# Optimization experiments

Measured on AMD Instinct MI355X. Metric: run time of the kernel, lower is better.

The kernel has to match this reference:

```python
import jax, jax.numpy as jnp
import numpy as np

B, T, V, E, DC, H = 128, 25, 10000, 512, 512, 512
N0 = H + E + DC  # layer-0 concat width
N1 = 2 * H       # layer-1 concat width


def setup_inputs() -> dict:
    key = jax.random.key(0)
    ks = jax.random.split(key, 12)
    def w(k, n):
        return jax.random.normal(k, (n, H), dtype=jnp.float32) / np.float32(np.sqrt(n))
    return {
        "tokens": jax.random.randint(ks[0], (B, T), 0, V),
        "processed_cnn_features": jax.random.normal(ks[1], (B, DC), dtype=jnp.float32),
        "initial_hidden_state": jnp.zeros((2, B, H), dtype=jnp.float32),
        "embedding": jax.random.normal(ks[2], (V, E), dtype=jnp.float32) * 0.1,
        "Wu0": w(ks[3], N0), "Wr0": w(ks[4], N0), "Wc0": w(ks[5], N0),
        "bu0": jnp.zeros((H,), jnp.float32), "br0": jnp.zeros((H,), jnp.float32), "bc0": jnp.zeros((H,), jnp.float32),
        "Wu1": w(ks[6], N1), "Wr1": w(ks[7], N1), "Wc1": w(ks[8], N1),
        "bu1": jnp.zeros((H,), jnp.float32), "br1": jnp.zeros((H,), jnp.float32), "bc1": jnp.zeros((H,), jnp.float32),
        "Wout": jax.random.normal(ks[9], (H, V), dtype=jnp.float32) / np.float32(np.sqrt(H)),
        "bout": jnp.zeros((V,), jnp.float32),
    }


def gru_step(x, h, Wu, bu, Wr, br, Wc, bc):
    xh = jnp.concatenate([x, h], axis=1)
    u = jax.nn.sigmoid(xh @ Wu + bu)
    r = jax.nn.sigmoid(xh @ Wr + br)
    cand = jnp.tanh(jnp.concatenate([x, r * h], axis=1) @ Wc + bc)
    return u * h + (1.0 - u) * cand


def reference(tokens, processed_cnn_features, initial_hidden_state, embedding,
              Wu0, Wr0, Wc0, bu0, br0, bc0,
              Wu1, Wr1, Wc1, bu1, br1, bc1,
              Wout, bout):
    emb = embedding[tokens]              # [B, T, E]
    emb_t = jnp.transpose(emb, (1, 0, 2))  # [T, B, E]

    def step(carry, e_t):
        h0, h1 = carry
        x0 = jnp.concatenate([e_t, processed_cnn_features], axis=1)  # [B, E+DC]
        h0 = gru_step(x0, h0, Wu0, bu0, Wr0, br0, Wc0, bc0)
        h1 = gru_step(h0, h1, Wu1, bu1, Wr1, br1, Wc1, bc1)
        logits = h1 @ Wout + bout  # [B, V]
        return (h0, h1), logits

    (h0, h1), logits_seq = jax.lax.scan(step, (initial_hidden_state[0], initial_hidden_state[1]), emb_t)
    logits = jnp.transpose(logits_seq, (1, 0, 2))  # [B, T, V]
    final_hidden = jnp.stack([h0, h1])             # [2, B, H]
    return logits, final_hidden
```

## Files before the change

### kernel.cpp

```cpp
#include <hip/hip_runtime.h>

#define T_ 25
#define V_ 10000
#define NWG_ 192

#define R_P3 0
#define R_P1 1
#define R_P4 2
#define R_P2 3

typedef short bf16x8 __attribute__((ext_vector_type(8)));
typedef float f32x4 __attribute__((ext_vector_type(4)));

__device__ __forceinline__ short f2bf(float x) {
  union { float f; unsigned u; } v; v.f = x;
  unsigned r = (v.u + 0x7fffu + ((v.u >> 16) & 1u)) >> 16;
  return (short)r;
}
__device__ __forceinline__ float sigm(float z) { return 1.f / (1.f + __expf(-z)); }
__device__ __forceinline__ float tanhfast(float z) {
  float e = __expf(2.f * z);
  return 1.f - 2.f / (e + 1.f);
}

__device__ __forceinline__ void gload_lds16(const void* g, void* l) {
  __builtin_amdgcn_global_load_lds((const __attribute__((address_space(1))) void*)g,
                                   (__attribute__((address_space(3))) void*)l, 16, 0, 0);
}

__device__ __forceinline__ void vwait0() { asm volatile("s_waitcnt vmcnt(0)" ::: "memory"); }
__device__ __forceinline__ void vwait_n(int n) {
  switch (n) {
    case 0:  asm volatile("s_waitcnt vmcnt(0)"  ::: "memory"); break;
    case 8:  asm volatile("s_waitcnt vmcnt(8)"  ::: "memory"); break;
    case 16: asm volatile("s_waitcnt vmcnt(16)" ::: "memory"); break;
    default: asm volatile("s_waitcnt vmcnt(0)"  ::: "memory"); break;
  }
}
__device__ __forceinline__ void ncload16(bf16x8* d, const short* p) {
  asm volatile("global_load_dwordx4 %0, %1, off" : "=v"(*d) : "v"(p) : "memory");
}
__device__ __forceinline__ void cstoref(float* p, float v) {
  asm volatile("global_store_dword %0, %1, off sc0 sc1" :: "v"(p), "v"(v) : "memory");
}
__device__ __forceinline__ void cstores(short* p, int v) {
  asm volatile("global_store_short %0, %1, off sc0 sc1" :: "v"(p), "v"(v) : "memory");
}

__device__ __forceinline__ int FL(int row, int col) {
  return (((col >> 5) * 8 + (row >> 4)) << 9) | (((row & 15) | (((col >> 3) & 3) << 4)) << 3) | (col & 7);
}

__device__ __forceinline__ void setflag(int* bar, int role, int wg, int val) {
  vwait0();
  __syncthreads();
  if (threadIdx.x == 0) {
    int* wp = bar + role * 256 + wg;
    asm volatile("global_store_dword %0, %1, off sc0 sc1" :: "v"(wp), "v"(val) : "memory");
  }
}
__device__ __forceinline__ void waitflag(int* bar, int role, int cnt, int need) {
  if (threadIdx.x < 64) {
    int idx = (int)threadIdx.x < cnt ? (int)threadIdx.x : cnt - 1;
    const int* wp = bar + role * 256 + idx;
    for (;;) {
      int v;
      asm volatile("global_load_dword %0, %1, off sc0 sc1" : "=v"(v) : "v"(wp) : "memory");
      asm volatile("s_waitcnt vmcnt(0)" ::: "memory");
      if (__all(v >= need)) break;
      __builtin_amdgcn_s_sleep(1);
    }
  }
  __syncthreads();
}

struct TJob { const float* src; short* dst; int R, C, t0; };
struct TJobs { TJob j[10]; };

__global__ void tcast_all(TJobs J) {
  __shared__ float t[32][33];
  int bid = blockIdx.x;
  int ji = 0;
  while (ji < 9 && bid >= J.j[ji + 1].t0) ji++;
  const float* src = J.j[ji].src;
  short* dst = J.j[ji].dst;
  int R = J.j[ji].R, C = J.j[ji].C;
  int rel = bid - J.j[ji].t0;
  int ctiles = (C + 31) >> 5;
  int rt0 = (rel / ctiles) * 32, ct0 = (rel % ctiles) * 32;
  int tx = threadIdx.x, ty = threadIdx.y;
#pragma unroll
  for (int i = 0; i < 4; i++) {
    int r = rt0 + ty + i * 8, c = ct0 + tx;
    if (r < R && c < C) t[ty + i * 8][tx] = src[(size_t)r * C + c];
  }
  __syncthreads();
#pragma unroll
  for (int i = 0; i < 4; i++) {
    int c = ct0 + ty + i * 8, r = rt0 + tx;
    if (r < R && c < C) dst[(size_t)c * R + r] = f2bf(t[tx][ty + i * 8]);
  }
}

__global__ void build_x0(const int* __restrict__ tok, const float* __restrict__ emb,
                         const float* __restrict__ cnn, short* __restrict__ X0) {
  int row = blockIdx.x;
  int t = row >> 7, b = row & 127;
  int tk = tok[b * T_ + t];
  const float* er = emb + (size_t)tk * 512;
  short* dst = X0 + (size_t)row * 1024;
  for (int i = threadIdx.x; i < 1024; i += 256)
    dst[i] = f2bf(i < 512 ? er[i] : cnn[b * 512 + (i - 512)]);
}

__global__ void init_h(const float* __restrict__ ihs, float* h0f0, float* h1f0, short* H0) {
  int i = blockIdx.x * 256 + threadIdx.x;
  if (i < 65536) {
    int b = i >> 9, h = i & 511;
    float v0 = ihs[i], v1 = ihs[65536 + i];
    h0f0[i] = v0; h1f0[i] = v1;
    H0[FL(b, h)] = f2bf(v0);
    H0[FL(b, 512 + h)] = f2bf(v1);
  }
}

struct RP {
  short *Hb, *XCb, *RHb, *H1all;
  float *u0b, *u1b, *h0b, *h1b;
  const float *A0;
  const short *Whur0T, *Whc0T, *W1urT, *Wc1T;
  const float *bu1, *br1, *bc1;
  float *outp;
  int *bar;
};

template<int NKS>
__device__ __forceinline__ void wload(const short* __restrict__ Wt, int n0, int lane, bf16x8* wfr) {
  const short* p = Wt + (size_t)(n0 + (lane & 15)) * (NKS * 32) + ((lane >> 4) * 8);
#pragma unroll
  for (int ks = 0; ks < NKS; ks++) wfr[ks] = *(const bf16x8*)(p + (size_t)ks * 32);
}

template<int NKS, bool SPLIT>
__device__ __forceinline__ void kcompute(const short* __restrict__ Alo, const short* __restrict__ Ahi,
                                         int rb0, int lane, const bf16x8* __restrict__ wfr, f32x4* acc) {
  const short* aplo = Alo + rb0 * 512 + lane * 8;
  const short* aphi = Ahi + rb0 * 512 + lane * 8;
  constexpr int NCH = NKS / 4;
  constexpr int DEPTH = NCH < 3 ? NCH : 3;
  bf16x8 s0[4][4], s1[4][4];
#pragma unroll
  for (int c = 0; c < DEPTH; c++)
#pragma unroll
    for (int j = 0; j < 4; j++) {
      int ks = c * 4 + j;
      const short* ap = (SPLIT && ks >= NKS / 2) ? aphi : aplo;
      ncload16(&s0[c & 3][j], ap + ks * 4096);
      ncload16(&s1[c & 3][j], ap + ks * 4096 + 512);
    }
#pragma unroll
  for (int c = 0; c < NCH; c++) {
    const int issued = (DEPTH + c < NCH) ? DEPTH + c : NCH;
    vwait_n((issued - c - 1) * 8);
    __builtin_amdgcn_sched_barrier(0);
#pragma unroll
    for (int j = 0; j < 4; j++) {
      int ks = c * 4 + j;
      acc[ks & 1]       = __builtin_amdgcn_mfma_f32_16x16x32_bf16(s0[c & 3][j], wfr[ks], acc[ks & 1], 0, 0, 0);
      acc[2 + (ks & 1)] = __builtin_amdgcn_mfma_f32_16x16x32_bf16(s1[c & 3][j], wfr[ks], acc[2 + (ks & 1)], 0, 0, 0);
    }
    if (DEPTH + c < NCH) {
      const int nc = DEPTH + c;
#pragma unroll
      for (int j = 0; j < 4; j++) {
        int ks = nc * 4 + j;
        const short* ap = (SPLIT && ks >= NKS / 2) ? aphi : aplo;
        ncload16(&s0[nc & 3][j], ap + ks * 4096);
        ncload16(&s1[nc & 3][j], ap + ks * 4096 + 512);
      }
    }
  }
}

__global__ __launch_bounds__(256, 1) void recurrence(RP p) {
  const int bid = blockIdx.x;
  const int m8 = bid & 7;
  const int k = ((bid & 127) >> 3) * 4 + (m8 & 3);
  const int role = (bid < 128) ? ((m8 < 4) ? R_P3 : R_P1) : ((m8 < 4) ? R_P4 : R_P2);
  const int tid = threadIdx.x, wv = tid >> 6, lane = tid & 63;
  const int lr = lane & 15, lg = lane >> 4;
  int* bar = p.bar;
  const int nt = k >> 1, mh = k & 1;
  const int colb = nt * 32 + (wv & 1) * 16;
  const int rb0 = mh * 4 + (wv >> 1) * 2;
  const int col = colb + lr;

  if (role == R_P3) {
    bf16x8 wfr[32]; wload<32>(p.W1urT, colb, lane, wfr);
    for (int s = 0; s < T_; s++) {
      waitflag(bar, R_P2, 32, s + 1);
      if (s >= 1) waitflag(bar, R_P4, 32, s);
      const short* Hs1 = p.Hb + (size_t)(s + 1) * 131072;
      const short* Hs  = p.Hb + (size_t)s * 131072;
      f32x4 acc[4] = {};
      kcompute<32, true>(Hs1, Hs, rb0, lane, wfr, acc);
      f32x4 am[2] = { acc[0] + acc[1], acc[2] + acc[3] };
      short* xc = p.XCb + (size_t)s * 131072;
      const float* h1s = p.h1b + (size_t)s * 65536;
      float* u1s = p.u1b + (size_t)s * 65536;
#pragma unroll
      for (int m = 0; m < 2; m++)
#pragma unroll
        for (int i = 0; i < 4; i++) {
          int row = (rb0 + m) * 16 + lg * 4 + i;
          if (colb < 512) {
            cstoref(&u1s[row * 512 + col], sigm(am[m][i] + p.bu1[col]));
          } else {
            float sg = sigm(am[m][i] + p.br1[col - 512]);
            cstores(&xc[FL(row, col)], f2bf(sg * h1s[row * 512 + (col - 512)]));
          }
        }
      setflag(bar, R_P3, k, s + 1);
    }
  } else if (role == R_P1) {
    bf16x8 wfr[16]; wload<16>(p.Whur0T, colb, lane, wfr);
    for (int s = 0; s < T_; s++) {
      if (s >= 1) waitflag(bar, R_P2, 32, s);
      const short* Hs = p.Hb + (size_t)s * 131072;
      f32x4 acc[4] = {};
      kcompute<16, false>(Hs, Hs, rb0, lane, wfr, acc);
      f32x4 am[2] = { acc[0] + acc[1], acc[2] + acc[3] };
      const float* a0s = p.A0 + (size_t)s * 196608;
      const float* h0s = p.h0b + (size_t)s * 65536;
      float* u0s = p.u0b + (size_t)s * 65536;
      short* rh = p.RHb + (size_t)s * 65536;
#pragma unroll
      for (int m = 0; m < 2; m++)
#pragma unroll
        for (int i = 0; i < 4; i++) {
          int row = (rb0 + m) * 16 + lg * 4 + i;
          if (colb < 512) {
            cstoref(&u0s[row * 512 + col], sigm(am[m][i] + a0s[row * 1536 + col]));
          } else {
            float sg = sigm(am[m][i] + a0s[row * 1536 + col]);
            cstores(&rh[FL(row, col - 512)], f2bf(sg * h0s[row * 512 + (col - 512)]));
          }
        }
      setflag(bar, R_P1, k, s + 1);
    }
  } else if (role == R_P4) {
    bf16x8 wfr[32]; wload<32>(p.Wc1T, colb, lane, wfr);
    for (int s = 0; s < T_; s++) {
      waitflag(bar, R_P3, 64, s + 1);
      waitflag(bar, R_P2, 32, s + 1);
      const short* xc = p.XCb + (size_t)s * 131072;
      f32x4 acc[4] = {};
      kcompute<32, false>(xc, xc, rb0, lane, wfr, acc);
      f32x4 am[2] = { acc[0] + acc[1], acc[2] + acc[3] };
      const float* u1s = p.u1b + (size_t)s * 65536;
      const float* h1s = p.h1b + (size_t)s * 65536;
      float* h1d = p.h1b + (size_t)(s + 1) * 65536;
      short* xh = p.Hb + (size_t)(s + 1) * 131072;
#pragma unroll
      for (int m = 0; m < 2; m++)
#pragma unroll
        for (int i = 0; i < 4; i++) {
          int row = (rb0 + m) * 16 + lg * 4 + i;
          float cc = tanhfast(am[m][i] + p.bc1[col]);
          float u = u1s[row * 512 + col], h = h1s[row * 512 + col];
          float hn = u * h + (1.f - u) * cc;
          cstoref(&h1d[row * 512 + col], hn);
          short hb = f2bf(hn);
          cstores(&xh[FL(row, 512 + col)], hb);
          p.H1all[(size_t)s * 65536 + row * 512 + col] = hb;
          if (s == T_ - 1) p.outp[32000000 + 65536 + row * 512 + col] = hn;
        }
      setflag(bar, R_P4, k, s + 1);
    }
  } else {
    bf16x8 wfr[16]; wload<16>(p.Whc0T, colb, lane, wfr);
    for (int s = 0; s < T_; s++) {
      waitflag(bar, R_P1, 64, s + 1);
      const short* rh = p.RHb + (size_t)s * 65536;
      f32x4 acc[4] = {};
      kcompute<16, false>(rh, rh, rb0, lane, wfr, acc);
      f32x4 am[2] = { acc[0] + acc[1], acc[2] + acc[3] };
      const float* a0s = p.A0 + (size_t)s * 196608;
      const float* u0s = p.u0b + (size_t)s * 65536;
      const float* h0s = p.h0b + (size_t)s * 65536;
      float* h0d = p.h0b + (size_t)(s + 1) * 65536;
      short* xh  = p.Hb + (size_t)(s + 1) * 131072;
      short* xcw = p.XCb + (size_t)s * 131072;
#pragma unroll
      for (int m = 0; m < 2; m++)
#pragma unroll
        for (int i = 0; i < 4; i++) {
          int row = (rb0 + m) * 16 + lg * 4 + i;
          float c = tanhfast(am[m][i] + a0s[row * 1536 + 1024 + col]);
          float u = u0s[row * 512 + col], h = h0s[row * 512 + col];
          float hn = u * h + (1.f - u) * c;
          cstoref(&h0d[row * 512 + col], hn);
          short hb = f2bf(hn);
          cstores(&xh[FL(row, col)], hb);
          cstores(&xcw[FL(row, col)], hb);
          if (s == T_ - 1) p.outp[32000000 + row * 512 + col] = hn;
        }
      setflag(bar, R_P2, k, s + 1);
    }
  }
}

struct GP {
  const short* A; const short* Bt;
  int lda, ldb, N, K;
  const float* bias0; const float* bias1; const float* bias2;
  float* fdst;
  float* outp; const float* bout;
};

template<int BM, int BN, int VAR>
__device__ __forceinline__ void gemm_core(const GP& p, short* la, short* lb, int bm, int bn, short* smem) {
  const int tid = threadIdx.x;
  const int wave = tid >> 6, lane = tid & 63;
  const int wm = wave >> 1, wn = wave & 1;
  constexpr int WM = BM / 2, WN = BN / 2;
  constexpr int MF = WM / 16, NF = WN / 16;
  const int lr = lane & 15, lg = lane >> 4;
  const short* Abase = p.A + (size_t)bm * BM * p.lda;
  const short* Bbase = p.Bt + (size_t)bn * BN * p.ldb;
  const int bnmax = p.N - bn * BN;
  f32x4 acc[MF][NF] = {};
  const int nkb = p.K >> 6;

  auto stA = [&](int buf, int k0) {
    constexpr int NI = BM / 32;
#pragma unroll
    for (int j = 0; j < NI; j++) {
      int glin = j * 256 + tid;
      int row = glin >> 3, gc = glin & 7;
      int gcs = gc ^ (row & 7);
      gload_lds16(Abase + (size_t)row * p.lda + k0 + gcs * 8,
                  &la[buf * BM * 64 + j * 2048 + wave * 512]);
    }
  };
  auto stB = [&](int buf, int k0) {
    constexpr int NI = BN / 32;
#pragma unroll
    for (int j = 0; j < NI; j++) {
      int glin = j * 256 + tid;
      int row = glin >> 3, gc = glin & 7;
      int gcs = gc ^ (row & 7);
      int rc = row < bnmax ? row : bnmax - 1;
      gload_lds16(Bbase + (size_t)rc * p.ldb + k0 + gcs * 8,
                  &lb[buf * BN * 64 + j * 2048 + wave * 512]);
    }
  };

  stA(0, 0); stB(0, 0);
  __syncthreads();
  int buf = 0;
  for (int kb = 0; kb < nkb; kb++) {
    if (kb + 1 < nkb) { stA(buf ^ 1, (kb + 1) * 64); stB(buf ^ 1, (kb + 1) * 64); }
    bf16x8 af[2][MF], bfr[2][NF];
#pragma unroll
    for (int ks = 0; ks < 2; ks++) {
#pragma unroll
      for (int m = 0; m < MF; m++) {
        int ar = wm * WM + m * 16 + lr;
        af[ks][m] = *(const bf16x8*)&la[buf * BM * 64 + (ar * 8 + ((ks * 4 + lg) ^ (ar & 7))) * 8];
      }
#pragma unroll
      for (int n = 0; n < NF; n++) {
        int br = wn * WN + n * 16 + lr;
        bfr[ks][n] = *(const bf16x8*)&lb[buf * BN * 64 + (br * 8 + ((ks * 4 + lg) ^ (br & 7))) * 8];
      }
    }
#pragma unroll
    for (int ks = 0; ks < 2; ks++)
#pragma unroll
      for (int m = 0; m < MF; m++)
#pragma unroll
        for (int n = 0; n < NF; n++)
          acc[m][n] = __builtin_amdgcn_mfma_f32_16x16x32_bf16(af[ks][m], bfr[ks][n], acc[m][n], 0, 0, 0);
    __syncthreads();
    buf ^= 1;
  }

  if constexpr (VAR == 0) {
#pragma unroll
    for (int m = 0; m < MF; m++)
#pragma unroll
      for (int n = 0; n < NF; n++)
#pragma unroll
        for (int i = 0; i < 4; i++) {
          int row = bm * BM + wm * WM + m * 16 + lg * 4 + i;
          int col = bn * BN + wn * WN + n * 16 + lr;
          if (col >= p.N) continue;
          float bias = col < 512 ? p.bias0[col] : (col < 1024 ? p.bias1[col - 512] : p.bias2[col - 1024]);
          p.fdst[(size_t)row * 1536 + col] = acc[m][n][i] + bias;
        }
  } else {
    float* fs = (float*)smem;
#pragma unroll
    for (int m = 0; m < MF; m++)
#pragma unroll
      for (int n = 0; n < NF; n++)
#pragma unroll
        for (int i = 0; i < 4; i++) {
          int lrow = wm * WM + m * 16 + lg * 4 + i;
          int lcol = wn * WN + n * 16 + lr;
          int col = bn * BN + lcol;
          fs[lrow * 128 + lcol] = acc[m][n][i] + (col < p.N ? p.bout[col] : 0.f);
        }
    __syncthreads();
#pragma unroll
    for (int j = 0; j < 16; j++) {
      int idx = j * 256 + tid;
      int r = idx >> 5, c4 = (idx & 31) << 2;
      int gr = bm * BM + r;
      int tt = gr >> 7, b = gr & 127;
      int col = bn * BN + c4;
      if (col < p.N) {
        f32x4 v = *(const f32x4*)&fs[r * 128 + c4];
        *(f32x4*)&p.outp[((size_t)b * T_ + tt) * V_ + col] = v;
      }
    }
  }
}

template<int BM, int BN, int VAR>
__global__ __launch_bounds__(256) void gemm_one(GP p) {
  __shared__ short smem[2 * BM * 64 + 2 * BN * 64];
  int bm, bn;
  if constexpr (VAR == 5) {
    int lin = blockIdx.y * gridDim.x + blockIdx.x;
    const int nwg = 79 * 25, q = nwg / 8, r8 = nwg % 8;
    int xcd = lin % 8, idx = lin / 8;
    int nlin = (xcd < r8 ? xcd * (q + 1) : r8 * (q + 1) + (xcd - r8) * q) + idx;
    bm = nlin % 25; bn = nlin / 25;
  } else { bm = blockIdx.y; bn = blockIdx.x; }
  gemm_core<BM, BN, VAR>(p, smem, smem + 2 * BM * 64, bm, bn, smem);
}

extern "C" void kernel_launch(void* const* d_in, const int* in_sizes, int n_in,
                              void* d_out, int out_size, void* d_ws, size_t ws_size,
                              hipStream_t stream) {
  const int*   tokens = (const int*)  d_in[0];
  const float* cnn    = (const float*)d_in[1];
  const float* ihs    = (const float*)d_in[2];
  const float* emb    = (const float*)d_in[3];
  const float* Wu0 = (const float*)d_in[4];
  const float* Wr0 = (const float*)d_in[5];
  const float* Wc0 = (const float*)d_in[6];
  const float* bu0 = (const float*)d_in[7];
  const float* br0 = (const float*)d_in[8];
  const float* bc0 = (const float*)d_in[9];
  const float* Wu1 = (const float*)d_in[10];
  const float* Wr1 = (const float*)d_in[11];
  const float* Wc1 = (const float*)d_in[12];
  const float* bu1 = (const float*)d_in[13];
  const float* br1 = (const float*)d_in[14];
  const float* bc1 = (const float*)d_in[15];
  const float* Wout = (const float*)d_in[16];
  const float* bout = (const float*)d_in[17];
  float* out = (float*)d_out;

  char* w = (char*)d_ws;
  size_t off = 0;
  auto alloc = [&](size_t bytes) { void* p = w + off; off += (bytes + 255) & ~255ull; return p; };
  short* WxT    = (short*)alloc(1536 * 1024 * 2);
  short* Whur0T = (short*)alloc(1024 * 512 * 2);
  short* Whc0T  = (short*)alloc(512 * 512 * 2);
  short* W1urT  = (short*)alloc(1024 * 1024 * 2);
  short* Wc1T   = (short*)alloc(512 * 1024 * 2);
  short* WoutT  = (short*)alloc((size_t)10000 * 512 * 2);
  short* X0     = (short*)alloc((size_t)3200 * 1024 * 2);
  float* A0     = (float*)alloc((size_t)3200 * 1536 * 4);
  short* H1all  = (short*)alloc((size_t)3200 * 512 * 2);
  short* Hb     = (short*)alloc((size_t)26 * 131072 * 2);
  short* XCb    = (short*)alloc((size_t)25 * 131072 * 2);
  short* RHb    = (short*)alloc((size_t)25 * 65536 * 2);
  float* u0b    = (float*)alloc((size_t)25 * 65536 * 4);
  float* u1b    = (float*)alloc((size_t)25 * 65536 * 4);
  float* h0b    = (float*)alloc((size_t)26 * 65536 * 4);
  float* h1b    = (float*)alloc((size_t)26 * 65536 * 4);
  int*   bar    = (int*)alloc(4096);
  (void)ws_size; (void)in_sizes; (void)n_in; (void)out_size;

  {
    TJobs J;
    J.j[0] = { Wu0,              WxT,                1024, 512,  0    };
    J.j[1] = { Wr0,              WxT + 512 * 1024,   1024, 512,  512  };
    J.j[2] = { Wc0,              WxT + 1024 * 1024,  1024, 512,  1024 };
    J.j[3] = { Wu0 + 1024 * 512, Whur0T,             512,  512,  1536 };
    J.j[4] = { Wr0 + 1024 * 512, Whur0T + 512 * 512, 512,  512,  1792 };
    J.j[5] = { Wc0 + 1024 * 512, Whc0T,              512,  512,  2048 };
    J.j[6] = { Wu1,              W1urT,              1024, 512,  2304 };
    J.j[7] = { Wr1,              W1urT + 512 * 1024, 1024, 512,  2816 };
    J.j[8] = { Wc1,              Wc1T,               1024, 512,  3328 };
    J.j[9] = { Wout,             WoutT,              512,  10000, 3840 };
    tcast_all<<<8848, dim3(32, 8), 0, stream>>>(J);
  }

  build_x0<<<3200, 256, 0, stream>>>(tokens, emb, cnn, X0);
  init_h<<<256, 256, 0, stream>>>(ihs, h0b, h1b, Hb);
  hipMemsetAsync(bar, 0, 4096, stream);

  {
    GP g = {};
    g.A = X0; g.lda = 1024; g.Bt = WxT; g.ldb = 1024; g.N = 1536; g.K = 1024;
    g.bias0 = bu0; g.bias1 = br0; g.bias2 = bc0; g.fdst = A0;
    gemm_one<128, 128, 0><<<dim3(12, 25), 256, 0, stream>>>(g);
  }

  {
    RP r = {};
    r.Hb = Hb; r.XCb = XCb; r.RHb = RHb; r.H1all = H1all;
    r.u0b = u0b; r.u1b = u1b; r.h0b = h0b; r.h1b = h1b;
    r.A0 = A0;
    r.Whur0T = Whur0T; r.Whc0T = Whc0T; r.W1urT = W1urT; r.Wc1T = Wc1T;
    r.bu1 = bu1; r.br1 = br1; r.bc1 = bc1;
    r.outp = out;
    r.bar = bar;
    recurrence<<<dim3(NWG_), 256, 0, stream>>>(r);
  }

  {
    GP g = {};
    g.A = H1all; g.lda = 512; g.Bt = WoutT; g.ldb = 512; g.N = 10000; g.K = 512;
    g.outp = out; g.bout = bout;
    gemm_one<128, 128, 5><<<dim3(79, 25), 256, 0, stream>>>(g);
  }
}
```

Measured before the change: 585.3 us.

## Fuse output projection GEMM into persistent recurrence kernel with per-step flags

Adds 64 extra workgroups to the persistent recurrence kernel. They compute the vocabulary projection tile by tile, each one waiting on the layer-1 step flag so the logits GEMM overlaps the sequential recurrence. The separate output GEMM launch is removed, and H1all stores become coherent stores so the consumer blocks can see them. In exchange, only 64 workgroups do the large projection instead of a full grid, and the recurrence kernel now carries a large LDS allocation.

```diff
diff --git a/kernel.cpp b/kernel.cpp
--- a/kernel.cpp
+++ b/kernel.cpp
@@ -2,7 +2,7 @@
 
 #define T_ 25
 #define V_ 10000
-#define NWG_ 192
+#define NWG_ 256
 
 #define R_P3 0
 #define R_P1 1
@@ -124,12 +124,138 @@
   }
 }
 
+struct GP {
+  const short* A; const short* Bt;
+  int lda, ldb, N, K;
+  const float* bias0; const float* bias1; const float* bias2;
+  float* fdst;
+  float* outp; const float* bout;
+};
+
+template<int BM, int BN, int VAR>
+__device__ __forceinline__ void gemm_core(const GP& p, short* la, short* lb, int bm, int bn, short* smem) {
+  const int tid = threadIdx.x;
+  const int wave = tid >> 6, lane = tid & 63;
+  const int wm = wave >> 1, wn = wave & 1;
+  constexpr int WM = BM / 2, WN = BN / 2;
+  constexpr int MF = WM / 16, NF = WN / 16;
+  const int lr = lane & 15, lg = lane >> 4;
+  const short* Abase = p.A + (size_t)bm * BM * p.lda;
+  const short* Bbase = p.Bt + (size_t)bn * BN * p.ldb;
+  const int bnmax = p.N - bn * BN;
+  f32x4 acc[MF][NF] = {};
+  const int nkb = p.K >> 6;
+
+  auto stA = [&](int buf, int k0) {
+    constexpr int NI = BM / 32;
+#pragma unroll
+    for (int j = 0; j < NI; j++) {
+      int glin = j * 256 + tid;
+      int row = glin >> 3, gc = glin & 7;
+      int gcs = gc ^ (row & 7);
+      gload_lds16(Abase + (size_t)row * p.lda + k0 + gcs * 8,
+                  &la[buf * BM * 64 + j * 2048 + wave * 512]);
+    }
+  };
+  auto stB = [&](int buf, int k0) {
+    constexpr int NI = BN / 32;
+#pragma unroll
+    for (int j = 0; j < NI; j++) {
+      int glin = j * 256 + tid;
+      int row = glin >> 3, gc = glin & 7;
+      int gcs = gc ^ (row & 7);
+      int rc = row < bnmax ? row : bnmax - 1;
+      gload_lds16(Bbase + (size_t)rc * p.ldb + k0 + gcs * 8,
+                  &lb[buf * BN * 64 + j * 2048 + wave * 512]);
+    }
+  };
+
+  stA(0, 0); stB(0, 0);
+  __syncthreads();
+  int buf = 0;
+  for (int kb = 0; kb < nkb; kb++) {
+    if (kb + 1 < nkb) { stA(buf ^ 1, (kb + 1) * 64); stB(buf ^ 1, (kb + 1) * 64); }
+    bf16x8 af[2][MF], bfr[2][NF];
+#pragma unroll
+    for (int ks = 0; ks < 2; ks++) {
+#pragma unroll
+      for (int m = 0; m < MF; m++) {
+        int ar = wm * WM + m * 16 + lr;
+        af[ks][m] = *(const bf16x8*)&la[buf * BM * 64 + (ar * 8 + ((ks * 4 + lg) ^ (ar & 7))) * 8];
+      }
+#pragma unroll
+      for (int n = 0; n < NF; n++) {
+        int br = wn * WN + n * 16 + lr;
+        bfr[ks][n] = *(const bf16x8*)&lb[buf * BN * 64 + (br * 8 + ((ks * 4 + lg) ^ (br & 7))) * 8];
+      }
+    }
+#pragma unroll
+    for (int ks = 0; ks < 2; ks++)
+#pragma unroll
+      for (int m = 0; m < MF; m++)
+#pragma unroll
+        for (int n = 0; n < NF; n++)
+          acc[m][n] = __builtin_amdgcn_mfma_f32_16x16x32_bf16(af[ks][m], bfr[ks][n], acc[m][n], 0, 0, 0);
+    __syncthreads();
+    buf ^= 1;
+  }
+
+  if constexpr (VAR == 0) {
+#pragma unroll
+    for (int m = 0; m < MF; m++)
+#pragma unroll
+      for (int n = 0; n < NF; n++)
+#pragma unroll
+        for (int i = 0; i < 4; i++) {
+          int row = bm * BM + wm * WM + m * 16 + lg * 4 + i;
+          int col = bn * BN + wn * WN + n * 16 + lr;
+          if (col >= p.N) continue;
+          float bias = col < 512 ? p.bias0[col] : (col < 1024 ? p.bias1[col - 512] : p.bias2[col - 1024]);
+          p.fdst[(size_t)row * 1536 + col] = acc[m][n][i] + bias;
+        }
+  } else {
+    float* fs = (float*)smem;
+#pragma unroll
+    for (int m = 0; m < MF; m++)
+#pragma unroll
+      for (int n = 0; n < NF; n++)
+#pragma unroll
+        for (int i = 0; i < 4; i++) {
+          int lrow = wm * WM + m * 16 + lg * 4 + i;
+          int lcol = wn * WN + n * 16 + lr;
+          int col = bn * BN + lcol;
+          fs[lrow * 128 + lcol] = acc[m][n][i] + (col < p.N ? p.bout[col] : 0.f);
+        }
+    __syncthreads();
+#pragma unroll
+    for (int j = 0; j < 16; j++) {
+      int idx = j * 256 + tid;
+      int r = idx >> 5, c4 = (idx & 31) << 2;
+      int gr = bm * BM + r;
+      int tt = gr >> 7, b = gr & 127;
+      int col = bn * BN + c4;
+      if (col < p.N) {
+        f32x4 v = *(const f32x4*)&fs[r * 128 + c4];
+        *(f32x4*)&p.outp[((size_t)b * T_ + tt) * V_ + col] = v;
+      }
+    }
+    __syncthreads();
+  }
+}
+
+template<int BM, int BN, int VAR>
+__global__ __launch_bounds__(256) void gemm_one(GP p) {
+  __shared__ short smem[2 * BM * 64 + 2 * BN * 64];
+  gemm_core<BM, BN, VAR>(p, smem, smem + 2 * BM * 64, blockIdx.y, blockIdx.x, smem);
+}
+
 struct RP {
   short *Hb, *XCb, *RHb, *H1all;
   float *u0b, *u1b, *h0b, *h1b;
   const float *A0;
   const short *Whur0T, *Whc0T, *W1urT, *Wc1T;
   const float *bu1, *br1, *bc1;
+  const short *WoutT; const float *bout;
   float *outp;
   int *bar;
 };
@@ -183,13 +309,29 @@
 }
 
 __global__ __launch_bounds__(256, 1) void recurrence(RP p) {
+  __shared__ short smem[2 * 128 * 64 + 2 * 128 * 64];
   const int bid = blockIdx.x;
+  int* bar = p.bar;
+  const int tid = threadIdx.x, wv = tid >> 6, lane = tid & 63;
+  const int lr = lane & 15, lg = lane >> 4;
+
+  if (bid >= 192) {
+    const int w = bid - 192;
+    GP g = {};
+    g.A = p.H1all; g.lda = 512; g.Bt = p.WoutT; g.ldb = 512; g.N = V_; g.K = 512;
+    g.outp = p.outp; g.bout = p.bout;
+    int done_t = 0;
+    for (int idx = w; idx < 79 * 25; idx += 64) {
+      int t = idx / 79, bn = idx % 79;
+      if (t + 1 > done_t) { waitflag(bar, R_P4, 32, t + 1); done_t = t + 1; }
+      gemm_core<128, 128, 5>(g, smem, smem + 2 * 128 * 64, t, bn, smem);
+    }
+    return;
+  }
+
   const int m8 = bid & 7;
   const int k = ((bid & 127) >> 3) * 4 + (m8 & 3);
   const int role = (bid < 128) ? ((m8 < 4) ? R_P3 : R_P1) : ((m8 < 4) ? R_P4 : R_P2);
-  const int tid = threadIdx.x, wv = tid >> 6, lane = tid & 63;
-  const int lr = lane & 15, lg = lane >> 4;
-  int* bar = p.bar;
   const int nt = k >> 1, mh = k & 1;
   const int colb = nt * 32 + (wv & 1) * 16;
   const int rb0 = mh * 4 + (wv >> 1) * 2;
@@ -272,7 +414,7 @@
           cstoref(&h1d[row * 512 + col], hn);
           short hb = f2bf(hn);
           cstores(&xh[FL(row, 512 + col)], hb);
-          p.H1all[(size_t)s * 65536 + row * 512 + col] = hb;
+          cstores(&p.H1all[(size_t)s * 65536 + row * 512 + col], hb);
           if (s == T_ - 1) p.outp[32000000 + 65536 + row * 512 + col] = hn;
         }
       setflag(bar, R_P4, k, s + 1);
@@ -308,138 +450,6 @@
       setflag(bar, R_P2, k, s + 1);
     }
   }
-}
-
-struct GP {
-  const short* A; const short* Bt;
-  int lda, ldb, N, K;
-  const float* bias0; const float* bias1; const float* bias2;
-  float* fdst;
-  float* outp; const float* bout;
-};
-
-template<int BM, int BN, int VAR>
-__device__ __forceinline__ void gemm_core(const GP& p, short* la, short* lb, int bm, int bn, short* smem) {
-  const int tid = threadIdx.x;
-  const int wave = tid >> 6, lane = tid & 63;
-  const int wm = wave >> 1, wn = wave & 1;
-  constexpr int WM = BM / 2, WN = BN / 2;
-  constexpr int MF = WM / 16, NF = WN / 16;
-  const int lr = lane & 15, lg = lane >> 4;
-  const short* Abase = p.A + (size_t)bm * BM * p.lda;
-  const short* Bbase = p.Bt + (size_t)bn * BN * p.ldb;
-  const int bnmax = p.N - bn * BN;
-  f32x4 acc[MF][NF] = {};
-  const int nkb = p.K >> 6;
-
-  auto stA = [&](int buf, int k0) {
-    constexpr int NI = BM / 32;
-#pragma unroll
-    for (int j = 0; j < NI; j++) {
-      int glin = j * 256 + tid;
-      int row = glin >> 3, gc = glin & 7;
-      int gcs = gc ^ (row & 7);
-      gload_lds16(Abase + (size_t)row * p.lda + k0 + gcs * 8,
-                  &la[buf * BM * 64 + j * 2048 + wave * 512]);
-    }
-  };
-  auto stB = [&](int buf, int k0) {
-    constexpr int NI = BN / 32;
-#pragma unroll
-    for (int j = 0; j < NI; j++) {
-      int glin = j * 256 + tid;
-      int row = glin >> 3, gc = glin & 7;
-      int gcs = gc ^ (row & 7);
-      int rc = row < bnmax ? row : bnmax - 1;
-      gload_lds16(Bbase + (size_t)rc * p.ldb + k0 + gcs * 8,
-                  &lb[buf * BN * 64 + j * 2048 + wave * 512]);
-    }
-  };
-
-  stA(0, 0); stB(0, 0);
-  __syncthreads();
-  int buf = 0;
-  for (int kb = 0; kb < nkb; kb++) {
-    if (kb + 1 < nkb) { stA(buf ^ 1, (kb + 1) * 64); stB(buf ^ 1, (kb + 1) * 64); }
-    bf16x8 af[2][MF], bfr[2][NF];
-#pragma unroll
-    for (int ks = 0; ks < 2; ks++) {
-#pragma unroll
-      for (int m = 0; m < MF; m++) {
-        int ar = wm * WM + m * 16 + lr;
-        af[ks][m] = *(const bf16x8*)&la[buf * BM * 64 + (ar * 8 + ((ks * 4 + lg) ^ (ar & 7))) * 8];
-      }
-#pragma unroll
-      for (int n = 0; n < NF; n++) {
-        int br = wn * WN + n * 16 + lr;
-        bfr[ks][n] = *(const bf16x8*)&lb[buf * BN * 64 + (br * 8 + ((ks * 4 + lg) ^ (br & 7))) * 8];
-      }
-    }
-#pragma unroll
-    for (int ks = 0; ks < 2; ks++)
-#pragma unroll
-      for (int m = 0; m < MF; m++)
-#pragma unroll
-        for (int n = 0; n < NF; n++)
-          acc[m][n] = __builtin_amdgcn_mfma_f32_16x16x32_bf16(af[ks][m], bfr[ks][n], acc[m][n], 0, 0, 0);
-    __syncthreads();
-    buf ^= 1;
-  }
-
-  if constexpr (VAR == 0) {
-#pragma unroll
-    for (int m = 0; m < MF; m++)
-#pragma unroll
-      for (int n = 0; n < NF; n++)
-#pragma unroll
-        for (int i = 0; i < 4; i++) {
-          int row = bm * BM + wm * WM + m * 16 + lg * 4 + i;
-          int col = bn * BN + wn * WN + n * 16 + lr;
-          if (col >= p.N) continue;
-          float bias = col < 512 ? p.bias0[col] : (col < 1024 ? p.bias1[col - 512] : p.bias2[col - 1024]);
-          p.fdst[(size_t)row * 1536 + col] = acc[m][n][i] + bias;
-        }
-  } else {
-    float* fs = (float*)smem;
-#pragma unroll
-    for (int m = 0; m < MF; m++)
-#pragma unroll
-      for (int n = 0; n < NF; n++)
-#pragma unroll
-        for (int i = 0; i < 4; i++) {
-          int lrow = wm * WM + m * 16 + lg * 4 + i;
-          int lcol = wn * WN + n * 16 + lr;
-          int col = bn * BN + lcol;
-          fs[lrow * 128 + lcol] = acc[m][n][i] + (col < p.N ? p.bout[col] : 0.f);
-        }
-    __syncthreads();
-#pragma unroll
-    for (int j = 0; j < 16; j++) {
-      int idx = j * 256 + tid;
-      int r = idx >> 5, c4 = (idx & 31) << 2;
-      int gr = bm * BM + r;
-      int tt = gr >> 7, b = gr & 127;
-      int col = bn * BN + c4;
-      if (col < p.N) {
-        f32x4 v = *(const f32x4*)&fs[r * 128 + c4];
-        *(f32x4*)&p.outp[((size_t)b * T_ + tt) * V_ + col] = v;
-      }
-    }
-  }
-}
-
-template<int BM, int BN, int VAR>
-__global__ __launch_bounds__(256) void gemm_one(GP p) {
-  __shared__ short smem[2 * BM * 64 + 2 * BN * 64];
-  int bm, bn;
-  if constexpr (VAR == 5) {
-    int lin = blockIdx.y * gridDim.x + blockIdx.x;
-    const int nwg = 79 * 25, q = nwg / 8, r8 = nwg % 8;
-    int xcd = lin % 8, idx = lin / 8;
-    int nlin = (xcd < r8 ? xcd * (q + 1) : r8 * (q + 1) + (xcd - r8) * q) + idx;
-    bm = nlin % 25; bn = nlin / 25;
-  } else { bm = blockIdx.y; bn = blockIdx.x; }
-  gemm_core<BM, BN, VAR>(p, smem, smem + 2 * BM * 64, bm, bn, smem);
 }
 
 extern "C" void kernel_launch(void* const* d_in, const int* in_sizes, int n_in,
@@ -520,15 +530,9 @@
     r.A0 = A0;
     r.Whur0T = Whur0T; r.Whc0T = Whc0T; r.W1urT = W1urT; r.Wc1T = Wc1T;
     r.bu1 = bu1; r.br1 = br1; r.bc1 = bc1;
+    r.WoutT = WoutT; r.bout = bout;
     r.outp = out;
     r.bar = bar;
     recurrence<<<dim3(NWG_), 256, 0, stream>>>(r);
   }
-
-  {
-    GP g = {};
-    g.A = H1all; g.lda = 512; g.Bt = WoutT; g.ldb = 512; g.N = 10000; g.K = 512;
-    g.outp = out; g.bout = bout;
-    gemm_one<128, 128, 5><<<dim3(79, 25), 256, 0, stream>>>(g);
-  }
-}
+}
```

Measured after the change: 521.2 us (median of 2 runs). 10.9% less time.
